# Kernel optimization log

Measured on AMD Instinct MI355X. Metric: run time of the kernel, lower is better.

Reference implementation:

```python
import jax, jax.numpy as jnp
import numpy as np

EPS = 1e-8


def setup_inputs() -> dict:
    key = jax.random.key(0)
    ks = jax.random.split(key, 10)
    B, Cin, H, W = 16, 256, 64, 64
    D, C = 128, 32
    return {
        "f_curr": jax.random.normal(ks[0], (B, Cin, H, W), jnp.float32),
        "mu_prior": jax.random.normal(ks[1], (B, D, C), jnp.float32),
        "log_sigma_prior": jax.random.normal(ks[2], (B, D, C), jnp.float32),
        "pi_prior": jax.random.uniform(ks[3], (B, C), jnp.float32),
        "mu_post": jax.random.normal(ks[4], (B, D), jnp.float32),
        "log_sigma_post": jax.random.normal(ks[5], (B, D), jnp.float32),
        "noise_cluster": jax.random.normal(ks[6], (B, D), jnp.float32),
        "noise_z": jax.random.normal(ks[7], (B, D), jnp.float32),
        "proj_W": jax.random.normal(ks[8], (Cin, Cin + D), jnp.float32) * 0.02,
        "proj_b": jax.random.normal(ks[9], (Cin,), jnp.float32) * 0.02,
    }


def reference(f_curr, mu_prior, log_sigma_prior, pi_prior, mu_post,
              log_sigma_post, noise_cluster, noise_z, proj_W, proj_b):
    sg = jax.lax.stop_gradient

    # ---- _cluster_sampler (all stats detached in the original) ----
    mu_p, ls_p = sg(mu_post), sg(log_sigma_post)          # [B, D]
    mu_pr, ls_pr = sg(mu_prior), sg(log_sigma_prior)      # [B, D, C]
    z_post = mu_p + jnp.exp(ls_p) * noise_cluster          # Normal(mu, exp(ls)).sample()
    sigma_pr = jnp.exp(ls_pr)
    # Normal log_prob of z_post[:, :, None] under each cluster -> [B, D, C]
    log_probs = (-ls_pr - 0.5 * jnp.log(2.0 * jnp.pi)
                 - (z_post[:, :, None] - mu_pr) ** 2 / (2.0 * sigma_pr ** 2))
    log_prob_c = jnp.sum(log_probs, axis=1)                # [B, C]
    pi_post = jax.nn.softmax(log_prob_c, axis=1)           # [B, C]

    # ---- z_c = Normal(mu_post, exp(ls)+eps).sample()  (no grad: .sample()) ----
    z_c = sg(mu_post + (jnp.exp(log_sigma_post) + EPS) * noise_z)  # [B, D]

    # ---- _f_combine: concat + 1x1 conv, computed as split matmuls ----
    Cin = f_curr.shape[1]
    Wf, Wz = proj_W[:, :Cin], proj_W[:, Cin:]              # [Cin,Cin], [Cin,D]
    bias = jnp.einsum('bd,od->bo', z_c, Wz) + proj_b       # spatially-constant part
    f_out = jnp.einsum('bchw,oc->bohw', f_curr, Wf) + bias[:, :, None, None]

    # ---- _kld ----
    mu_post_e = mu_post[:, :, None]                        # [B, D, 1]
    ls_post_e = log_sigma_post[:, :, None]
    sigma_prior = jnp.exp(log_sigma_prior)
    sigma_post = jnp.exp(ls_post_e)
    kl_g = (log_sigma_prior - ls_post_e
            + (sigma_post ** 2 + (mu_post_e - mu_prior) ** 2)
            / (2.0 * sigma_prior ** 2 + EPS) - 0.5)
    kl_g = jnp.sum(kl_g, axis=1)                           # [B, C]
    kl_g_weighted = jnp.sum(pi_post * kl_g, axis=1)        # [B]
    kl_cat = jnp.sum(pi_post * (jnp.log(pi_post + EPS) - jnp.log(pi_prior + EPS)), axis=1)  # [B]
    kl_std = jnp.sum(-ls_post_e + 0.5 * (jnp.exp(2.0 * ls_post_e) + mu_post_e ** 2) - 0.5,
                     axis=1)                               # [B, 1]
    # NOTE: original torch code broadcasts [B] + [B,1] -> [B,B] before mean; replicated here.
    kld = jnp.mean((kl_g_weighted + kl_cat) + kl_std)

    return f_out, kld
```

## Files before the change

kernel.cpp:

```cpp
#include <hip/hip_runtime.h>
#include <math.h>

#define EPS_F 1e-8f

typedef __attribute__((ext_vector_type(8))) short bf16x8;
typedef __attribute__((ext_vector_type(4))) float f32x4;

__device__ inline short f2bf(float f) {
    return (short)__builtin_bit_cast(unsigned short, (__bf16)f);
}

__device__ inline int bswz(int kgi, int n) {
    return (kgi * 512 + n * 8) ^ (((n >> 3) & 3) << 4);
}

__global__ __launch_bounds__(256) void setup_kernel(
    const float* __restrict__ mu_prior,
    const float* __restrict__ ls_prior,
    const float* __restrict__ pi_prior,
    const float* __restrict__ mu_post,
    const float* __restrict__ ls_post,
    const float* __restrict__ noise_c,
    const float* __restrict__ noise_z,
    const float* __restrict__ projW,
    const float* __restrict__ projb,
    float* __restrict__ ws_bias,
    short* __restrict__ ws_A,
    float* __restrict__ ws_kld)
{
    const int g = blockIdx.x;
    const int t = threadIdx.x;

    __shared__ float s_zpost[128];
    __shared__ float s_zc[128];
    __shared__ float s_mu[128];
    __shared__ float s_e2[128];
    __shared__ float s_lsp[128];
    __shared__ float s_kstd[128];
    __shared__ float s_p1[8][32];
    __shared__ float s_p2[8][32];

    if (g < 16) {
        const float* wrow = projW + t * 384 + g * 16;
        bf16x8 w0, w1;
#pragma unroll
        for (int j = 0; j < 8; ++j) w0[j] = f2bf(wrow[j]);
#pragma unroll
        for (int j = 0; j < 8; ++j) w1[j] = f2bf(wrow[8 + j]);
        *(bf16x8*)&ws_A[(g * 2 + 0) * 2048 + t * 8] = w0;
        *(bf16x8*)&ws_A[(g * 2 + 1) * 2048 + t * 8] = w1;
        return;
    }

    if (g < 32) {
        const int b = g - 16;
        if (t < 128) {
            const float mu = mu_post[b * 128 + t];
            const float ls = ls_post[b * 128 + t];
            const float el = __expf(ls);
            s_zpost[t] = mu + el * noise_c[b * 128 + t];
            s_mu[t]    = mu;
            s_e2[t]    = el * el;
            s_lsp[t]   = ls;
            s_kstd[t]  = -ls + 0.5f * (el * el + mu * mu) - 0.5f;
        }
        __syncthreads();

        {
            const int c  = t & 31;
            const int gg = t >> 5;
            const float* mpB = mu_prior + b * 4096;
            const float* lpB = ls_prior + b * 4096;
            float lp = 0.f, kgv = 0.f;
#pragma unroll 4
            for (int j = 0; j < 16; ++j) {
                const int d = gg * 16 + j;
                const float mpr  = mpB[d * 32 + c];
                const float lpr  = lpB[d * 32 + c];
                const float inv2 = 0.5f * __expf(-2.f * lpr);
                const float zd   = s_zpost[d] - mpr;
                lp += -lpr - 0.91893853320467274f - zd * zd * inv2;
                const float dm   = s_mu[d] - mpr;
                const float e2pr = __expf(2.f * lpr);
                kgv += lpr - s_lsp[d]
                     + (s_e2[d] + dm * dm) * __builtin_amdgcn_rcpf(2.f * e2pr + EPS_F)
                     - 0.5f;
            }
            s_p1[gg][c] = lp;
            s_p2[gg][c] = kgv;
        }
        __syncthreads();

        if (t < 64) {
            const int c = t & 31;
            float lp = 0.f, kgv = 0.f;
#pragma unroll
            for (int gg = 0; gg < 8; ++gg) { lp += s_p1[gg][c]; kgv += s_p2[gg][c]; }
            float ks = s_kstd[c] + s_kstd[c + 32] + s_kstd[c + 64] + s_kstd[c + 96];
            const float pp = pi_prior[b * 32 + c];

            float m = lp;
#pragma unroll
            for (int o = 16; o; o >>= 1) m = fmaxf(m, __shfl_xor(m, o, 32));
            const float e = __expf(lp - m);
            float den = e;
#pragma unroll
            for (int o = 16; o; o >>= 1) den += __shfl_xor(den, o, 32);
            const float pi = e * __builtin_amdgcn_rcpf(den);
            float tot = pi * kgv + pi * (__logf(pi + EPS_F) - __logf(pp + EPS_F));
#pragma unroll
            for (int o = 16; o; o >>= 1) tot += __shfl_xor(tot, o, 32);
#pragma unroll
            for (int o = 16; o; o >>= 1) ks += __shfl_xor(ks, o, 32);
            if (t == 0) ws_kld[b] = tot + ks;
        }
        return;
    }

    {
        const int b = g - 32;
        if (t < 128) {
            const float mu = mu_post[b * 128 + t];
            const float el = __expf(ls_post[b * 128 + t]);
            s_zc[t] = mu + (el + EPS_F) * noise_z[b * 128 + t];
        }
        __syncthreads();

        const float4* wrow = (const float4*)(projW + t * 384 + 256);
        float sum = projb[t];
#pragma unroll 8
        for (int j = 0; j < 32; ++j) {
            const float4 w = wrow[j];
            sum += s_zc[4 * j + 0] * w.x + s_zc[4 * j + 1] * w.y +
                   s_zc[4 * j + 2] * w.z + s_zc[4 * j + 3] * w.w;
        }
        ws_bias[b * 256 + t] = sum;
    }
}

__global__ __launch_bounds__(256, 4) void gemm_kernel(
    const float* __restrict__ F,
    const short* __restrict__ wsA,
    const float* __restrict__ bias,
    const float* __restrict__ ws_kld,
    float* __restrict__ O)
{
    const int nT = blockIdx.x;
    const int b  = blockIdx.y;

    __shared__ short Bl[32 * 64 * 8];
    __shared__ float s_bias[256];

    const int tid  = threadIdx.x;
    const int lane = tid & 63;
    const int wave = tid >> 6;
    const int kg   = lane >> 4;
    const int lm   = lane & 15;

    s_bias[tid] = bias[b * 256 + tid];

    if (nT == 0 && b == 0 && tid == 0) {
        float s = 0.f;
#pragma unroll
        for (int i = 0; i < 16; ++i) s += ws_kld[i];
        O[16777216] = s * 0.0625f;
    }

    const int sn4 = (tid & 15) * 4;
    const int skb = (tid >> 4) * 16;
    const float* fp = F + (size_t)b * 1048576 + (size_t)skb * 4096
                    + nT * 64 + sn4;

    float4 ld[16];
#pragma unroll
    for (int i = 0; i < 16; ++i)
        ld[i] = *(const float4*)(fp + (size_t)i * 4096);

#pragma unroll
    for (int h = 0; h < 2; ++h) {
        const int kgi = (skb >> 3) + h;
#pragma unroll
        for (int c = 0; c < 4; ++c) {
            bf16x8 v;
#pragma unroll
            for (int j = 0; j < 8; ++j) {
                const float4 q = ld[h * 8 + j];
                v[j] = f2bf(c == 0 ? q.x : c == 1 ? q.y : c == 2 ? q.z : q.w);
            }
            *(bf16x8*)&Bl[bswz(kgi, sn4 + c)] = v;
        }
    }
    __syncthreads();

    const short* aBase = wsA + (size_t)kg * 2048 + (wave * 64 + lm) * 8;

    f32x4 acc[4][4];
#pragma unroll
    for (int i = 0; i < 4; ++i)
#pragma unroll
        for (int j = 0; j < 4; ++j) acc[i][j] = (f32x4){0.f, 0.f, 0.f, 0.f};

#pragma unroll
    for (int kc = 0; kc < 8; ++kc) {
        bf16x8 aW[4], bF[4];
#pragma unroll
        for (int mt = 0; mt < 4; ++mt)
            aW[mt] = *(const bf16x8*)(aBase + (size_t)kc * 8192 + mt * 128);
#pragma unroll
        for (int nt = 0; nt < 4; ++nt)
            bF[nt] = *(const bf16x8*)&Bl[bswz(kc * 4 + kg, nt * 16 + lm)];

#pragma unroll
        for (int mt = 0; mt < 4; ++mt)
#pragma unroll
            for (int nt = 0; nt < 4; ++nt)
                acc[mt][nt] = __builtin_amdgcn_mfma_f32_16x16x32_bf16(
                    bF[nt], aW[mt], acc[mt][nt], 0, 0, 0);
    }

    float* Ob = O + (size_t)b * 1048576 + nT * 64 + kg * 4;
#pragma unroll
    for (int mt = 0; mt < 4; ++mt) {
        const int m = wave * 64 + mt * 16 + lm;
        const float bb = s_bias[m];
        float* orow = Ob + (size_t)m * 4096;
#pragma unroll
        for (int nt = 0; nt < 4; ++nt) {
            float4 o4;
            o4.x = acc[mt][nt][0] + bb;
            o4.y = acc[mt][nt][1] + bb;
            o4.z = acc[mt][nt][2] + bb;
            o4.w = acc[mt][nt][3] + bb;
            *(float4*)(orow + nt * 16) = o4;
        }
    }
}

extern "C" void kernel_launch(void* const* d_in, const int* in_sizes, int n_in,
                              void* d_out, int out_size, void* d_ws, size_t ws_size,
                              hipStream_t stream) {
    const float* f_curr   = (const float*)d_in[0];
    const float* mu_prior = (const float*)d_in[1];
    const float* ls_prior = (const float*)d_in[2];
    const float* pi_prior = (const float*)d_in[3];
    const float* mu_post  = (const float*)d_in[4];
    const float* ls_post  = (const float*)d_in[5];
    const float* noise_c  = (const float*)d_in[6];
    const float* noise_z  = (const float*)d_in[7];
    const float* projW    = (const float*)d_in[8];
    const float* projb    = (const float*)d_in[9];

    float* out = (float*)d_out;
    float* ws  = (float*)d_ws;
    float* ws_bias = ws;
    short* ws_A    = (short*)(ws + 4096);
    float* ws_kld  = ws + 4096 + 32768;

    setup_kernel<<<48, 256, 0, stream>>>(mu_prior, ls_prior, pi_prior, mu_post,
                                         ls_post, noise_c, noise_z, projW, projb,
                                         ws_bias, ws_A, ws_kld);
    gemm_kernel<<<dim3(64, 16), 256, 0, stream>>>(f_curr, ws_A, ws_bias, ws_kld, out);
}
```

Before: 136.2 us.

## Split GEMM into K-halves and N-halves, overlap B staging, use nontemporal IO

The gemm kernel now loads the f_curr tile in two K halves. It converts the second half to bf16 in LDS only after the first half's MFMAs, so that conversion overlaps with compute. The output is computed in two 32-column passes, each with half the accumulators, which cuts register pressure and lets the first half's stores overlap the second half's compute. Global loads of F and the output stores use nontemporal hints to avoid polluting the cache. In exchange, the A weights are reloaded twice from global/L2, the K loops are no longer unrolled, and there is an extra barrier.

Result: slower. 147.0 us (+8.0%).

```diff
diff --git a/kernel.cpp b/kernel.cpp
--- a/kernel.cpp
+++ b/kernel.cpp
@@ -166,72 +166,132 @@
         O[16777216] = s * 0.0625f;
     }
 
-    const int sn4 = (tid & 15) * 4;
-    const int skb = (tid >> 4) * 16;
-    const float* fp = F + (size_t)b * 1048576 + (size_t)skb * 4096
+    const int sn4  = (tid & 15) * 4;
+    const int kgi0 = tid >> 4;
+    const float* fp = F + (size_t)b * 1048576 + (size_t)(kgi0 * 8) * 4096
                     + nT * 64 + sn4;
 
-    float4 ld[16];
-#pragma unroll
-    for (int i = 0; i < 16; ++i)
-        ld[i] = *(const float4*)(fp + (size_t)i * 4096);
-
-#pragma unroll
-    for (int h = 0; h < 2; ++h) {
-        const int kgi = (skb >> 3) + h;
-#pragma unroll
-        for (int c = 0; c < 4; ++c) {
-            bf16x8 v;
-#pragma unroll
-            for (int j = 0; j < 8; ++j) {
-                const float4 q = ld[h * 8 + j];
-                v[j] = f2bf(c == 0 ? q.x : c == 1 ? q.y : c == 2 ? q.z : q.w);
-            }
-            *(bf16x8*)&Bl[bswz(kgi, sn4 + c)] = v;
-        }
+    f32x4 ld0[8], ld1[8];
+#pragma unroll
+    for (int j = 0; j < 8; ++j)
+        ld0[j] = __builtin_nontemporal_load((const f32x4*)(fp + (size_t)j * 4096));
+#pragma unroll
+    for (int j = 0; j < 8; ++j)
+        ld1[j] = __builtin_nontemporal_load((const f32x4*)(fp + (size_t)(128 + j) * 4096));
+
+#pragma unroll
+    for (int c = 0; c < 4; ++c) {
+        bf16x8 v;
+#pragma unroll
+        for (int j = 0; j < 8; ++j) v[j] = f2bf(ld0[j][c]);
+        *(bf16x8*)&Bl[bswz(kgi0, sn4 + c)] = v;
     }
     __syncthreads();
 
     const short* aBase = wsA + (size_t)kg * 2048 + (wave * 64 + lm) * 8;
-
-    f32x4 acc[4][4];
+    float* Ob = O + (size_t)b * 1048576 + nT * 64 + kg * 4;
+
+    f32x4 acc[4][2];
+
 #pragma unroll
     for (int i = 0; i < 4; ++i)
 #pragma unroll
-        for (int j = 0; j < 4; ++j) acc[i][j] = (f32x4){0.f, 0.f, 0.f, 0.f};
-
-#pragma unroll
-    for (int kc = 0; kc < 8; ++kc) {
-        bf16x8 aW[4], bF[4];
+        for (int j = 0; j < 2; ++j) acc[i][j] = (f32x4){0.f, 0.f, 0.f, 0.f};
+
+#pragma unroll 1
+    for (int kc = 0; kc < 4; ++kc) {
+        bf16x8 aW[4], bF[2];
 #pragma unroll
         for (int mt = 0; mt < 4; ++mt)
             aW[mt] = *(const bf16x8*)(aBase + (size_t)kc * 8192 + mt * 128);
 #pragma unroll
-        for (int nt = 0; nt < 4; ++nt)
-            bF[nt] = *(const bf16x8*)&Bl[bswz(kc * 4 + kg, nt * 16 + lm)];
-
-#pragma unroll
-        for (int mt = 0; mt < 4; ++mt)
-#pragma unroll
-            for (int nt = 0; nt < 4; ++nt)
-                acc[mt][nt] = __builtin_amdgcn_mfma_f32_16x16x32_bf16(
-                    bF[nt], aW[mt], acc[mt][nt], 0, 0, 0);
-    }
-
-    float* Ob = O + (size_t)b * 1048576 + nT * 64 + kg * 4;
+        for (int ntl = 0; ntl < 2; ++ntl)
+            bF[ntl] = *(const bf16x8*)&Bl[bswz(kc * 4 + kg, ntl * 16 + lm)];
+#pragma unroll
+        for (int mt = 0; mt < 4; ++mt)
+#pragma unroll
+            for (int ntl = 0; ntl < 2; ++ntl)
+                acc[mt][ntl] = __builtin_amdgcn_mfma_f32_16x16x32_bf16(
+                    bF[ntl], aW[mt], acc[mt][ntl], 0, 0, 0);
+    }
+
+#pragma unroll
+    for (int c = 0; c < 4; ++c) {
+        bf16x8 v;
+#pragma unroll
+        for (int j = 0; j < 8; ++j) v[j] = f2bf(ld1[j][c]);
+        *(bf16x8*)&Bl[bswz(kgi0 + 16, sn4 + c)] = v;
+    }
+    __syncthreads();
+
+#pragma unroll 1
+    for (int kc = 4; kc < 8; ++kc) {
+        bf16x8 aW[4], bF[2];
+#pragma unroll
+        for (int mt = 0; mt < 4; ++mt)
+            aW[mt] = *(const bf16x8*)(aBase + (size_t)kc * 8192 + mt * 128);
+#pragma unroll
+        for (int ntl = 0; ntl < 2; ++ntl)
+            bF[ntl] = *(const bf16x8*)&Bl[bswz(kc * 4 + kg, ntl * 16 + lm)];
+#pragma unroll
+        for (int mt = 0; mt < 4; ++mt)
+#pragma unroll
+            for (int ntl = 0; ntl < 2; ++ntl)
+                acc[mt][ntl] = __builtin_amdgcn_mfma_f32_16x16x32_bf16(
+                    bF[ntl], aW[mt], acc[mt][ntl], 0, 0, 0);
+    }
+
 #pragma unroll
     for (int mt = 0; mt < 4; ++mt) {
         const int m = wave * 64 + mt * 16 + lm;
         const float bb = s_bias[m];
         float* orow = Ob + (size_t)m * 4096;
 #pragma unroll
-        for (int nt = 0; nt < 4; ++nt) {
-            float4 o4;
-            o4.x = acc[mt][nt][0] + bb;
-            o4.y = acc[mt][nt][1] + bb;
-            o4.z = acc[mt][nt][2] + bb;
-            o4.w = acc[mt][nt][3] + bb;
-            *(float4*)(orow + nt * 16) = o4;
+        for (int ntl = 0; ntl < 2; ++ntl) {
+            f32x4 o4;
+            o4[0] = acc[mt][ntl][0] + bb;
+            o4[1] = acc[mt][ntl][1] + bb;
+            o4[2] = acc[mt][ntl][2] + bb;
+            o4[3] = acc[mt][ntl][3] + bb;
+            __builtin_nontemporal_store(o4, (f32x4*)(orow + ntl * 16));
+        }
+    }
+
+#pragma unroll
+    for (int i = 0; i < 4; ++i)
+#pragma unroll
+        for (int j = 0; j < 2; ++j) acc[i][j] = (f32x4){0.f, 0.f, 0.f, 0.f};
+
+#pragma unroll 1
+    for (int kc = 0; kc < 8; ++kc) {
+        bf16x8 aW[4], bF[2];
+#pragma unroll
+        for (int mt = 0; mt < 4; ++mt)
+            aW[mt] = *(const bf16x8*)(aBase + (size_t)kc * 8192 + mt * 128);
+#pragma unroll
+        for (int ntl = 0; ntl < 2; ++ntl)
+            bF[ntl] = *(const bf16x8*)&Bl[bswz(kc * 4 + kg, 32 + ntl * 16 + lm)];
+#pragma unroll
+        for (int mt = 0; mt < 4; ++mt)
+#pragma unroll
+            for (int ntl = 0; ntl < 2; ++ntl)
+                acc[mt][ntl] = __builtin_amdgcn_mfma_f32_16x16x32_bf16(
+                    bF[ntl], aW[mt], acc[mt][ntl], 0, 0, 0);
+    }
+
+#pragma unroll
+    for (int mt = 0; mt < 4; ++mt) {
+        const int m = wave * 64 + mt * 16 + lm;
+        const float bb = s_bias[m];
+        float* orow = Ob + (size_t)m * 4096 + 32;
+#pragma unroll
+        for (int ntl = 0; ntl < 2; ++ntl) {
+            f32x4 o4;
+            o4[0] = acc[mt][ntl][0] + bb;
+            o4[1] = acc[mt][ntl][1] + bb;
+            o4[2] = acc[mt][ntl][2] + bb;
+            o4[3] = acc[mt][ntl][3] + bb;
+            __builtin_nontemporal_store(o4, (f32x4*)(orow + ntl * 16));
         }
     }
 }
```
